# Optimization experiments

Hardware: AMD Instinct MI355X
Metric: run time of the kernel (lower is better)

## Reference

```python
import jax, jax.numpy as jnp
import numpy as np
from jax import lax

IN, H, OUT = 28, 64, 10


def _uniform(key, shape, bound):
    return jax.random.uniform(key, shape, jnp.float32, -bound, bound)


def setup_inputs() -> dict:
    key = jax.random.key(0)
    ks = jax.random.split(key, 11)
    b = 1.0 / np.sqrt(H)  # PyTorch LSTM/Linear init bound
    x = jax.random.normal(ks[0], (2048, 512, IN), jnp.float32)
    return {
        "x": x,
        "W_ih0": _uniform(ks[1], (4 * H, IN), b),
        "W_hh0": _uniform(ks[2], (4 * H, H), b),
        "b_ih0": _uniform(ks[3], (4 * H,), b),
        "b_hh0": _uniform(ks[4], (4 * H,), b),
        "W_ih1": _uniform(ks[5], (4 * H, H), b),
        "W_hh1": _uniform(ks[6], (4 * H, H), b),
        "b_ih1": _uniform(ks[7], (4 * H,), b),
        "b_hh1": _uniform(ks[8], (4 * H,), b),
        "W_out": _uniform(ks[9], (OUT, H), b),
        "b_out": _uniform(ks[10], (OUT,), b),
    }


def _lstm_layer(x_tbd, Wih, Whh, bih, bhh):
    # x_tbd: [T, B, D]; PyTorch gate order: i, f, g, o
    B = x_tbd.shape[1]
    h0 = jnp.zeros((B, H), x_tbd.dtype)
    c0 = jnp.zeros((B, H), x_tbd.dtype)
    bias = bih + bhh

    def step(carry, x_t):
        h, c = carry
        gates = x_t @ Wih.T + h @ Whh.T + bias  # [B, 4H]
        i, f, g, o = jnp.split(gates, 4, axis=-1)
        i = jax.nn.sigmoid(i)
        f = jax.nn.sigmoid(f)
        g = jnp.tanh(g)
        o = jax.nn.sigmoid(o)
        c = f * c + i * g
        h = o * jnp.tanh(c)
        return (h, c), h

    (_, _), hs = lax.scan(step, (h0, c0), x_tbd)
    return hs  # [T, B, H]


def reference(x, W_ih0, W_hh0, b_ih0, b_hh0, W_ih1, W_hh1, b_ih1, b_hh1, W_out, b_out):
    x_tbd = jnp.transpose(x, (1, 0, 2))  # [T, B, IN]
    h1 = _lstm_layer(x_tbd, W_ih0, W_hh0, b_ih0, b_hh0)  # [T, B, H]
    h2 = _lstm_layer(h1, W_ih1, W_hh1, b_ih1, b_hh1)     # [T, B, H]
    r_last = h2[-1]                                      # r_out[:, -1, :] -> [B, H]
    out = r_last @ W_out.T + b_out                       # [B, OUT]
    return out, r_last
```

## Files before the change

### kernel.cpp

```cpp
#include <hip/hip_runtime.h>
#include <stddef.h>

#define NT 512
#define NI 28
#define NH 64
#define BT 8
#define CH 16
#define XPh 36
#define HPh 72
#define NTH 512

typedef _Float16 f16x8 __attribute__((ext_vector_type(8)));
typedef float    f32x4 __attribute__((ext_vector_type(4)));

__device__ __forceinline__ float sigm(float v)  { return __builtin_amdgcn_rcpf(1.f + __expf(-v)); }
__device__ __forceinline__ float tanh_(float v) { return 1.f - 2.f * __builtin_amdgcn_rcpf(__expf(2.f * v) + 1.f); }

__device__ __forceinline__ void bar_lds() {
    asm volatile("s_waitcnt lgkmcnt(0)\n\ts_barrier" ::: "memory");
}

__device__ __forceinline__ size_t gxi(int idx, int n0, int b0) {
    int b   = idx / (CH * 7);
    int rem = idx - b * (CH * 7);
    int t   = rem / 7;
    int w7  = rem - t * 7;
    return ((size_t)(b0 + b) * NT + (n0 + t)) * 7 + w7;
}
__device__ __forceinline__ void xstoreh(_Float16* dst, int idx, float4 v) {
    int b   = idx / (CH * 7);
    int rem = idx - b * (CH * 7);
    int t   = rem / 7;
    int w7  = rem - t * 7;
    _Float16* row = dst + (t * BT + b) * XPh;
    _Float16 tmp[4] = { (_Float16)v.x, (_Float16)v.y, (_Float16)v.z, (_Float16)v.w };
    *(uint2*)(row + 4 * w7) = *(const uint2*)tmp;
}

__global__ __launch_bounds__(NTH, 2)
void lstm2_mfma(const float* __restrict__ x,
                const float* __restrict__ Wih0, const float* __restrict__ Whh0,
                const float* __restrict__ bih0, const float* __restrict__ bhh0,
                const float* __restrict__ Wih1, const float* __restrict__ Whh1,
                const float* __restrict__ bih1, const float* __restrict__ bhh1,
                const float* __restrict__ Wout, const float* __restrict__ bout,
                float* __restrict__ out, float* __restrict__ rlast)
{
    __shared__ __align__(16) _Float16 s_x[2][CH * BT * XPh];
    __shared__ __align__(16) _Float16 s_h0[2][BT * HPh];
    __shared__ __align__(16) _Float16 s_h1[2][BT * HPh];
    __shared__ __align__(16) float    s_hf[BT * NH];

    const int tid = threadIdx.x;
    const int ln  = tid & 63;
    const int wv  = tid >> 6;
    const int lay = wv >> 2;
    const int w4  = wv & 3;
    const int b0  = blockIdx.x * BT;

    const int colB = ln & 15;
    const int kq   = (ln >> 4) * 8;
    const int bA   = ln & 7;
    const int ue   = w4 * 16 + colB;
    const int m0   = (ln >> 4) * 4;
    const int rq   = (ln >= 32) ? 2 : 0;
    const int bm0  = (m0 + rq) & 7;
    const int bm1  = (m0 + rq + 1) & 7;
    const bool hi  = (rq != 0);
    const int off0 = bm0 * HPh + ue;
    const int off1 = bm1 * HPh + ue;

    #pragma unroll 1
    for (int i = tid; i < (int)(sizeof(s_x) / 4); i += NTH) ((int*)s_x)[i] = 0;
    #pragma unroll 1
    for (int i = tid; i < (int)((sizeof(s_h0) + sizeof(s_h1)) / 4); i += NTH) ((int*)s_h0)[i] = 0;
    __syncthreads();
    if (tid < 2 * CH * BT) {
        int buf = tid >> 7, r = tid & 127;
        s_x[buf][r * XPh + 28] = (_Float16)1.0f;
    }

    const float4* xg4 = (const float4*)x;
    {
        float4 v = xg4[gxi(tid, 0, b0)];
        xstoreh(s_x[0], tid, v);
        if (tid < 384) {
            float4 v2 = xg4[gxi(tid + NTH, 0, b0)];
            xstoreh(s_x[0], tid + NTH, v2);
        }
    }
    __syncthreads();

    const f32x4 z4 = { 0.f, 0.f, 0.f, 0.f };
    float cc0 = 0.f, cc1 = 0.f;
    float4 pfA, pfB;

    if (lay == 0) {
        f16x8 B0[4], B1[4], B2[4];
        #pragma unroll
        for (int t = 0; t < 4; ++t) {
            const int g = 64 * t + ue;
            const float bias0 = bih0[g] + bhh0[g];
            #pragma unroll
            for (int j = 0; j < 8; ++j) {
                int k = kq + j;
                float w0 = (k < NI) ? Wih0[g * NI + k] : (k == 28 ? bias0 : 0.f);
                B0[t][j] = (_Float16)w0;
                B1[t][j] = (_Float16)Whh0[g * NH + k];
                B2[t][j] = (_Float16)Whh0[g * NH + 32 + k];
            }
        }
        f32x4 accx[4];
        #pragma unroll 1
        for (int n = 0; n <= NT; ++n) {
            if ((n & 15) == 0 && n + CH < NT) {
                pfA = xg4[gxi(tid, n + CH, b0)];
                if (tid < 384) pfB = xg4[gxi(tid + NTH, n + CH, b0)];
            }
            if (n < NT) {
                if ((n & 15) == 0) {
                    const _Float16* xrow = s_x[(n >> 4) & 1] + ((n & 15) * BT + bA) * XPh;
                    f16x8 Ax = *(const f16x8*)(xrow + kq);
                    #pragma unroll
                    for (int t = 0; t < 4; ++t)
                        accx[t] = __builtin_amdgcn_mfma_f32_16x16x32_f16(Ax, B0[t], z4, 0, 0, 0);
                }
                const _Float16* h0r = s_h0[(n - 1) & 1] + bA * HPh;
                f16x8 A0 = *(const f16x8*)(h0r + kq);
                f16x8 A1 = *(const f16x8*)(h0r + 32 + kq);
                f32x4 acc[4];
                #pragma unroll
                for (int t = 0; t < 4; ++t) {
                    f32x4 a = __builtin_amdgcn_mfma_f32_16x16x32_f16(A0, B1[t], accx[t], 0, 0, 0);
                    acc[t]  = __builtin_amdgcn_mfma_f32_16x16x32_f16(A1, B2[t], a, 0, 0, 0);
                }
                float g00 = hi ? acc[0][2] : acc[0][0];
                float g10 = hi ? acc[1][2] : acc[1][0];
                float g20 = hi ? acc[2][2] : acc[2][0];
                float g30 = hi ? acc[3][2] : acc[3][0];
                float g01 = hi ? acc[0][3] : acc[0][1];
                float g11 = hi ? acc[1][3] : acc[1][1];
                float g21 = hi ? acc[2][3] : acc[2][1];
                float g31 = hi ? acc[3][3] : acc[3][1];
                _Float16* hw = s_h0[n & 1];
                cc0 = sigm(g10) * cc0 + sigm(g00) * tanh_(g20);
                hw[off0] = (_Float16)(sigm(g30) * tanh_(cc0));
                cc1 = sigm(g11) * cc1 + sigm(g01) * tanh_(g21);
                hw[off1] = (_Float16)(sigm(g31) * tanh_(cc1));
                if ((n & 15) != 15 && n + 1 < NT) {
                    const _Float16* xrow2 = s_x[((n + 1) >> 4) & 1] + (((n + 1) & 15) * BT + bA) * XPh;
                    f16x8 Ax2 = *(const f16x8*)(xrow2 + kq);
                    #pragma unroll
                    for (int t = 0; t < 4; ++t)
                        accx[t] = __builtin_amdgcn_mfma_f32_16x16x32_f16(Ax2, B0[t], z4, 0, 0, 0);
                }
            }
            if ((n & 15) == 15 && n + 1 < NT) {
                _Float16* dst = s_x[((n >> 4) + 1) & 1];
                xstoreh(dst, tid, pfA);
                if (tid < 384) xstoreh(dst, tid + NTH, pfB);
            }
            bar_lds();
        }
    } else {
        f16x8 B0[4], B1[4], B2[4], B3[4]; f32x4 bseed[4];
        #pragma unroll
        for (int t = 0; t < 4; ++t) {
            const int g = 64 * t + ue;
            const float bf = bih1[g] + bhh1[g];
            bseed[t] = (f32x4){ bf, bf, bf, bf };
            #pragma unroll
            for (int j = 0; j < 8; ++j) {
                int k = kq + j;
                B0[t][j] = (_Float16)Wih1[g * NH + k];
                B1[t][j] = (_Float16)Wih1[g * NH + 32 + k];
                B2[t][j] = (_Float16)Whh1[g * NH + k];
                B3[t][j] = (_Float16)Whh1[g * NH + 32 + k];
            }
        }
        #pragma unroll 1
        for (int n = 0; n <= NT; ++n) {
            if ((n & 15) == 0 && n + CH < NT) {
                pfA = xg4[gxi(tid, n + CH, b0)];
                if (tid < 384) pfB = xg4[gxi(tid + NTH, n + CH, b0)];
            }
            if (n >= 1) {
                const _Float16* h0r = s_h0[(n - 1) & 1] + bA * HPh;
                const _Float16* h1r = s_h1[n & 1] + bA * HPh;
                f16x8 A0 = *(const f16x8*)(h0r + kq);
                f16x8 A1 = *(const f16x8*)(h0r + 32 + kq);
                f16x8 A2 = *(const f16x8*)(h1r + kq);
                f16x8 A3 = *(const f16x8*)(h1r + 32 + kq);
                f32x4 accp[4], accq[4];
                #pragma unroll
                for (int t = 0; t < 4; ++t) {
                    f32x4 p = __builtin_amdgcn_mfma_f32_16x16x32_f16(A0, B0[t], bseed[t], 0, 0, 0);
                    accp[t] = __builtin_amdgcn_mfma_f32_16x16x32_f16(A1, B1[t], p, 0, 0, 0);
                    f32x4 q = __builtin_amdgcn_mfma_f32_16x16x32_f16(A2, B2[t], z4, 0, 0, 0);
                    accq[t] = __builtin_amdgcn_mfma_f32_16x16x32_f16(A3, B3[t], q, 0, 0, 0);
                }
                float g00 = (hi ? accp[0][2] : accp[0][0]) + (hi ? accq[0][2] : accq[0][0]);
                float g10 = (hi ? accp[1][2] : accp[1][0]) + (hi ? accq[1][2] : accq[1][0]);
                float g20 = (hi ? accp[2][2] : accp[2][0]) + (hi ? accq[2][2] : accq[2][0]);
                float g30 = (hi ? accp[3][2] : accp[3][0]) + (hi ? accq[3][2] : accq[3][0]);
                float g01 = (hi ? accp[0][3] : accp[0][1]) + (hi ? accq[0][3] : accq[0][1]);
                float g11 = (hi ? accp[1][3] : accp[1][1]) + (hi ? accq[1][3] : accq[1][1]);
                float g21 = (hi ? accp[2][3] : accp[2][1]) + (hi ? accq[2][3] : accq[2][1]);
                float g31 = (hi ? accp[3][3] : accp[3][1]) + (hi ? accq[3][3] : accq[3][1]);
                _Float16* hw = s_h1[(n - 1) & 1];
                cc0 = sigm(g10) * cc0 + sigm(g00) * tanh_(g20);
                float h0v = sigm(g30) * tanh_(cc0);
                hw[off0] = (_Float16)h0v;
                cc1 = sigm(g11) * cc1 + sigm(g01) * tanh_(g21);
                float h1v = sigm(g31) * tanh_(cc1);
                hw[off1] = (_Float16)h1v;
                if (n == NT) {
                    rlast[(size_t)(b0 + bm0) * NH + ue] = h0v;
                    rlast[(size_t)(b0 + bm1) * NH + ue] = h1v;
                    s_hf[bm0 * NH + ue] = h0v;
                    s_hf[bm1 * NH + ue] = h1v;
                }
            }
            if ((n & 15) == 15 && n + 1 < NT) {
                _Float16* dst = s_x[((n >> 4) + 1) & 1];
                xstoreh(dst, tid, pfA);
                if (tid < 384) xstoreh(dst, tid + NTH, pfB);
            }
            bar_lds();
        }
    }

    if (tid < BT * 10) {
        int b = tid / 10, o = tid - 10 * (tid / 10);
        float a = bout[o];
        #pragma unroll
        for (int u = 0; u < NH; ++u) a += Wout[o * NH + u] * s_hf[b * NH + u];
        out[(size_t)(b0 + b) * 10 + o] = a;
    }
}

extern "C" void kernel_launch(void* const* d_in, const int* in_sizes, int n_in,
                              void* d_out, int out_size, void* d_ws, size_t ws_size,
                              hipStream_t stream) {
    const float* x    = (const float*)d_in[0];
    const float* Wih0 = (const float*)d_in[1];
    const float* Whh0 = (const float*)d_in[2];
    const float* bih0 = (const float*)d_in[3];
    const float* bhh0 = (const float*)d_in[4];
    const float* Wih1 = (const float*)d_in[5];
    const float* Whh1 = (const float*)d_in[6];
    const float* bih1 = (const float*)d_in[7];
    const float* bhh1 = (const float*)d_in[8];
    const float* Wout = (const float*)d_in[9];
    const float* bout = (const float*)d_in[10];

    const int B = in_sizes[0] / (NT * NI);
    float* out   = (float*)d_out;
    float* rlast = out + (size_t)B * 10;

    dim3 grid(B / BT), block(NTH);
    hipLaunchKernelGGL(lstm2_mfma, grid, block, 0, stream,
                       x, Wih0, Whh0, bih0, bhh0, Wih1, Whh1, bih1, bhh1,
                       Wout, bout, out, rlast);
}
```

Before: 471.1 us.

## Halve batch tile to 4 rows per block and double blocks per CU

```diff
diff --git a/kernel.cpp b/kernel.cpp
--- a/kernel.cpp
+++ b/kernel.cpp
@@ -4,17 +4,22 @@
 #define NT 512
 #define NI 28
 #define NH 64
-#define BT 8
+#define BT 4
 #define CH 16
 #define XPh 36
 #define HPh 72
 #define NTH 512
+#define XLD (CH*BT*7)
 
 typedef _Float16 f16x8 __attribute__((ext_vector_type(8)));
 typedef float    f32x4 __attribute__((ext_vector_type(4)));
 
 __device__ __forceinline__ float sigm(float v)  { return __builtin_amdgcn_rcpf(1.f + __expf(-v)); }
 __device__ __forceinline__ float tanh_(float v) { return 1.f - 2.f * __builtin_amdgcn_rcpf(__expf(2.f * v) + 1.f); }
+
+__device__ __forceinline__ float sel4(f32x4 a, int q) {
+    return q == 0 ? a[0] : (q == 1 ? a[1] : (q == 2 ? a[2] : a[3]));
+}
 
 __device__ __forceinline__ void bar_lds() {
     asm volatile("s_waitcnt lgkmcnt(0)\n\ts_barrier" ::: "memory");
@@ -37,7 +42,7 @@
     *(uint2*)(row + 4 * w7) = *(const uint2*)tmp;
 }
 
-__global__ __launch_bounds__(NTH, 2)
+__global__ __launch_bounds__(NTH, 4)
 void lstm2_mfma(const float* __restrict__ x,
                 const float* __restrict__ Wih0, const float* __restrict__ Whh0,
                 const float* __restrict__ bih0, const float* __restrict__ bhh0,
@@ -59,16 +64,11 @@
     const int b0  = blockIdx.x * BT;
 
     const int colB = ln & 15;
-    const int kq   = (ln >> 4) * 8;
-    const int bA   = ln & 7;
+    const int q    = ln >> 4;
+    const int kq   = q * 8;
+    const int bA   = ln & 3;
     const int ue   = w4 * 16 + colB;
-    const int m0   = (ln >> 4) * 4;
-    const int rq   = (ln >= 32) ? 2 : 0;
-    const int bm0  = (m0 + rq) & 7;
-    const int bm1  = (m0 + rq + 1) & 7;
-    const bool hi  = (rq != 0);
-    const int off0 = bm0 * HPh + ue;
-    const int off1 = bm1 * HPh + ue;
+    const int offh = q * HPh + ue;
 
     #pragma unroll 1
     for (int i = tid; i < (int)(sizeof(s_x) / 4); i += NTH) ((int*)s_x)[i] = 0;
@@ -76,24 +76,20 @@
     for (int i = tid; i < (int)((sizeof(s_h0) + sizeof(s_h1)) / 4); i += NTH) ((int*)s_h0)[i] = 0;
     __syncthreads();
     if (tid < 2 * CH * BT) {
-        int buf = tid >> 7, r = tid & 127;
+        int buf = tid >> 6, r = tid & 63;
         s_x[buf][r * XPh + 28] = (_Float16)1.0f;
     }
 
     const float4* xg4 = (const float4*)x;
-    {
+    if (tid < XLD) {
         float4 v = xg4[gxi(tid, 0, b0)];
         xstoreh(s_x[0], tid, v);
-        if (tid < 384) {
-            float4 v2 = xg4[gxi(tid + NTH, 0, b0)];
-            xstoreh(s_x[0], tid + NTH, v2);
-        }
     }
     __syncthreads();
 
     const f32x4 z4 = { 0.f, 0.f, 0.f, 0.f };
-    float cc0 = 0.f, cc1 = 0.f;
-    float4 pfA, pfB;
+    float cc0 = 0.f;
+    float4 pfA;
 
     if (lay == 0) {
         f16x8 B0[4], B1[4], B2[4];
@@ -113,10 +109,8 @@
         f32x4 accx[4];
         #pragma unroll 1
         for (int n = 0; n <= NT; ++n) {
-            if ((n & 15) == 0 && n + CH < NT) {
+            if ((n & 15) == 0 && n + CH < NT && tid < XLD)
                 pfA = xg4[gxi(tid, n + CH, b0)];
-                if (tid < 384) pfB = xg4[gxi(tid + NTH, n + CH, b0)];
-            }
             if (n < NT) {
                 if ((n & 15) == 0) {
                     const _Float16* xrow = s_x[(n >> 4) & 1] + ((n & 15) * BT + bA) * XPh;
@@ -134,19 +128,12 @@
                     f32x4 a = __builtin_amdgcn_mfma_f32_16x16x32_f16(A0, B1[t], accx[t], 0, 0, 0);
                     acc[t]  = __builtin_amdgcn_mfma_f32_16x16x32_f16(A1, B2[t], a, 0, 0, 0);
                 }
-                float g00 = hi ? acc[0][2] : acc[0][0];
-                float g10 = hi ? acc[1][2] : acc[1][0];
-                float g20 = hi ? acc[2][2] : acc[2][0];
-                float g30 = hi ? acc[3][2] : acc[3][0];
-                float g01 = hi ? acc[0][3] : acc[0][1];
-                float g11 = hi ? acc[1][3] : acc[1][1];
-                float g21 = hi ? acc[2][3] : acc[2][1];
-                float g31 = hi ? acc[3][3] : acc[3][1];
-                _Float16* hw = s_h0[n & 1];
-                cc0 = sigm(g10) * cc0 + sigm(g00) * tanh_(g20);
-                hw[off0] = (_Float16)(sigm(g30) * tanh_(cc0));
-                cc1 = sigm(g11) * cc1 + sigm(g01) * tanh_(g21);
-                hw[off1] = (_Float16)(sigm(g31) * tanh_(cc1));
+                float g0 = sel4(acc[0], q);
+                float g1 = sel4(acc[1], q);
+                float g2 = sel4(acc[2], q);
+                float g3 = sel4(acc[3], q);
+                cc0 = sigm(g1) * cc0 + sigm(g0) * tanh_(g2);
+                s_h0[n & 1][offh] = (_Float16)(sigm(g3) * tanh_(cc0));
                 if ((n & 15) != 15 && n + 1 < NT) {
                     const _Float16* xrow2 = s_x[((n + 1) >> 4) & 1] + (((n + 1) & 15) * BT + bA) * XPh;
                     f16x8 Ax2 = *(const f16x8*)(xrow2 + kq);
@@ -155,11 +142,8 @@
                         accx[t] = __builtin_amdgcn_mfma_f32_16x16x32_f16(Ax2, B0[t], z4, 0, 0, 0);
                 }
             }
-            if ((n & 15) == 15 && n + 1 < NT) {
-                _Float16* dst = s_x[((n >> 4) + 1) & 1];
-                xstoreh(dst, tid, pfA);
-                if (tid < 384) xstoreh(dst, tid + NTH, pfB);
-            }
+            if ((n & 15) == 15 && n + 1 < NT && tid < XLD)
+                xstoreh(s_x[((n >> 4) + 1) & 1], tid, pfA);
             bar_lds();
         }
     } else {
@@ -180,10 +164,8 @@
         }
         #pragma unroll 1
         for (int n = 0; n <= NT; ++n) {
-            if ((n & 15) == 0 && n + CH < NT) {
+            if ((n & 15) == 0 && n + CH < NT && tid < XLD)
                 pfA = xg4[gxi(tid, n + CH, b0)];
-                if (tid < 384) pfB = xg4[gxi(tid + NTH, n + CH, b0)];
-            }
             if (n >= 1) {
                 const _Float16* h0r = s_h0[(n - 1) & 1] + bA * HPh;
                 const _Float16* h1r = s_h1[n & 1] + bA * HPh;
@@ -191,41 +173,28 @@
                 f16x8 A1 = *(const f16x8*)(h0r + 32 + kq);
                 f16x8 A2 = *(const f16x8*)(h1r + kq);
                 f16x8 A3 = *(const f16x8*)(h1r + 32 + kq);
-                f32x4 accp[4], accq[4];
+                f32x4 acc[4];
                 #pragma unroll
                 for (int t = 0; t < 4; ++t) {
-                    f32x4 p = __builtin_amdgcn_mfma_f32_16x16x32_f16(A0, B0[t], bseed[t], 0, 0, 0);
-                    accp[t] = __builtin_amdgcn_mfma_f32_16x16x32_f16(A1, B1[t], p, 0, 0, 0);
-                    f32x4 q = __builtin_amdgcn_mfma_f32_16x16x32_f16(A2, B2[t], z4, 0, 0, 0);
-                    accq[t] = __builtin_amdgcn_mfma_f32_16x16x32_f16(A3, B3[t], q, 0, 0, 0);
-                }
-                float g00 = (hi ? accp[0][2] : accp[0][0]) + (hi ? accq[0][2] : accq[0][0]);
-                float g10 = (hi ? accp[1][2] : accp[1][0]) + (hi ? accq[1][2] : accq[1][0]);
-                float g20 = (hi ? accp[2][2] : accp[2][0]) + (hi ? accq[2][2] : accq[2][0]);
-                float g30 = (hi ? accp[3][2] : accp[3][0]) + (hi ? accq[3][2] : accq[3][0]);
-                float g01 = (hi ? accp[0][3] : accp[0][1]) + (hi ? accq[0][3] : accq[0][1]);
-                float g11 = (hi ? accp[1][3] : accp[1][1]) + (hi ? accq[1][3] : accq[1][1]);
-                float g21 = (hi ? accp[2][3] : accp[2][1]) + (hi ? accq[2][3] : accq[2][1]);
-                float g31 = (hi ? accp[3][3] : accp[3][1]) + (hi ? accq[3][3] : accq[3][1]);
-                _Float16* hw = s_h1[(n - 1) & 1];
-                cc0 = sigm(g10) * cc0 + sigm(g00) * tanh_(g20);
-                float h0v = sigm(g30) * tanh_(cc0);
-                hw[off0] = (_Float16)h0v;
-                cc1 = sigm(g11) * cc1 + sigm(g01) * tanh_(g21);
-                float h1v = sigm(g31) * tanh_(cc1);
-                hw[off1] = (_Float16)h1v;
+                    f32x4 a = __builtin_amdgcn_mfma_f32_16x16x32_f16(A0, B0[t], bseed[t], 0, 0, 0);
+                    a       = __builtin_amdgcn_mfma_f32_16x16x32_f16(A1, B1[t], a, 0, 0, 0);
+                    a       = __builtin_amdgcn_mfma_f32_16x16x32_f16(A2, B2[t], a, 0, 0, 0);
+                    acc[t]  = __builtin_amdgcn_mfma_f32_16x16x32_f16(A3, B3[t], a, 0, 0, 0);
+                }
+                float g0 = sel4(acc[0], q);
+                float g1 = sel4(acc[1], q);
+                float g2 = sel4(acc[2], q);
+                float g3 = sel4(acc[3], q);
+                cc0 = sigm(g1) * cc0 + sigm(g0) * tanh_(g2);
+                float hv = sigm(g3) * tanh_(cc0);
+                s_h1[(n - 1) & 1][offh] = (_Float16)hv;
                 if (n == NT) {
-                    rlast[(size_t)(b0 + bm0) * NH + ue] = h0v;
-                    rlast[(size_t)(b0 + bm1) * NH + ue] = h1v;
-                    s_hf[bm0 * NH + ue] = h0v;
-                    s_hf[bm1 * NH + ue] = h1v;
-                }
-            }
-            if ((n & 15) == 15 && n + 1 < NT) {
-                _Float16* dst = s_x[((n >> 4) + 1) & 1];
-                xstoreh(dst, tid, pfA);
-                if (tid < 384) xstoreh(dst, tid + NTH, pfB);
-            }
+                    rlast[(size_t)(b0 + q) * NH + ue] = hv;
+                    s_hf[q * NH + ue] = hv;
+                }
+            }
+            if ((n & 15) == 15 && n + 1 < NT && tid < XLD)
+                xstoreh(s_x[((n >> 4) + 1) & 1], tid, pfA);
             bar_lds();
         }
     }
```

After: 609.0 us. 1.29x slower.

## Replace per-step block barriers with LDS flag spin-waits between LSTM layers

Applied to the files above, without the earlier changes.

```diff
diff --git a/kernel.cpp b/kernel.cpp
--- a/kernel.cpp
+++ b/kernel.cpp
@@ -9,16 +9,14 @@
 #define XPh 36
 #define HPh 72
 #define NTH 512
+#define XLD (CH*BT*7)
+#define LEAD 4
 
 typedef _Float16 f16x8 __attribute__((ext_vector_type(8)));
 typedef float    f32x4 __attribute__((ext_vector_type(4)));
 
 __device__ __forceinline__ float sigm(float v)  { return __builtin_amdgcn_rcpf(1.f + __expf(-v)); }
 __device__ __forceinline__ float tanh_(float v) { return 1.f - 2.f * __builtin_amdgcn_rcpf(__expf(2.f * v) + 1.f); }
-
-__device__ __forceinline__ void bar_lds() {
-    asm volatile("s_waitcnt lgkmcnt(0)\n\ts_barrier" ::: "memory");
-}
 
 __device__ __forceinline__ size_t gxi(int idx, int n0, int b0) {
     int b   = idx / (CH * 7);
@@ -47,9 +45,10 @@
                 float* __restrict__ out, float* __restrict__ rlast)
 {
     __shared__ __align__(16) _Float16 s_x[2][CH * BT * XPh];
-    __shared__ __align__(16) _Float16 s_h0[2][BT * HPh];
+    __shared__ __align__(16) _Float16 s_h0[LEAD][BT * HPh];
     __shared__ __align__(16) _Float16 s_h1[2][BT * HPh];
     __shared__ __align__(16) float    s_hf[BT * NH];
+    __shared__ __align__(16) int      s_fl[8];
 
     const int tid = threadIdx.x;
     const int ln  = tid & 63;
@@ -73,7 +72,10 @@
     #pragma unroll 1
     for (int i = tid; i < (int)(sizeof(s_x) / 4); i += NTH) ((int*)s_x)[i] = 0;
     #pragma unroll 1
-    for (int i = tid; i < (int)((sizeof(s_h0) + sizeof(s_h1)) / 4); i += NTH) ((int*)s_h0)[i] = 0;
+    for (int i = tid; i < (int)(sizeof(s_h0) / 4); i += NTH) ((int*)s_h0)[i] = 0;
+    #pragma unroll 1
+    for (int i = tid; i < (int)(sizeof(s_h1) / 4); i += NTH) ((int*)s_h1)[i] = 0;
+    if (tid < 8) s_fl[tid] = -1;
     __syncthreads();
     if (tid < 2 * CH * BT) {
         int buf = tid >> 7, r = tid & 127;
@@ -84,7 +86,7 @@
     {
         float4 v = xg4[gxi(tid, 0, b0)];
         xstoreh(s_x[0], tid, v);
-        if (tid < 384) {
+        if (tid < XLD - NTH) {
             float4 v2 = xg4[gxi(tid + NTH, 0, b0)];
             xstoreh(s_x[0], tid + NTH, v2);
         }
@@ -93,7 +95,8 @@
 
     const f32x4 z4 = { 0.f, 0.f, 0.f, 0.f };
     float cc0 = 0.f, cc1 = 0.f;
-    float4 pfA, pfB;
+    volatile int* fl0 = s_fl;
+    volatile int* fl1 = s_fl + 4;
 
     if (lay == 0) {
         f16x8 B0[4], B1[4], B2[4];
@@ -110,57 +113,70 @@
                 B2[t][j] = (_Float16)Whh0[g * NH + 32 + k];
             }
         }
+        float4 pf0, pf1, pf2, pf3;
         f32x4 accx[4];
         #pragma unroll 1
-        for (int n = 0; n <= NT; ++n) {
+        for (int n = 0; n < NT; ++n) {
             if ((n & 15) == 0 && n + CH < NT) {
-                pfA = xg4[gxi(tid, n + CH, b0)];
-                if (tid < 384) pfB = xg4[gxi(tid + NTH, n + CH, b0)];
-            }
-            if (n < NT) {
-                if ((n & 15) == 0) {
-                    const _Float16* xrow = s_x[(n >> 4) & 1] + ((n & 15) * BT + bA) * XPh;
-                    f16x8 Ax = *(const f16x8*)(xrow + kq);
-                    #pragma unroll
-                    for (int t = 0; t < 4; ++t)
-                        accx[t] = __builtin_amdgcn_mfma_f32_16x16x32_f16(Ax, B0[t], z4, 0, 0, 0);
-                }
-                const _Float16* h0r = s_h0[(n - 1) & 1] + bA * HPh;
-                f16x8 A0 = *(const f16x8*)(h0r + kq);
-                f16x8 A1 = *(const f16x8*)(h0r + 32 + kq);
-                f32x4 acc[4];
+                pf0 = xg4[gxi(tid,       n + CH, b0)];
+                pf1 = xg4[gxi(tid + 256, n + CH, b0)];
+                pf2 = xg4[gxi(tid + 512, n + CH, b0)];
+                if (tid < XLD - 768) pf3 = xg4[gxi(tid + 768, n + CH, b0)];
+            }
+            for (;;) {
+                int a0 = fl0[0], a1 = fl0[1], a2 = fl0[2], a3 = fl0[3];
+                int c0 = fl1[0], c1 = fl1[1], c2 = fl1[2], c3 = fl1[3];
+                int mn0 = min(min(a0, a1), min(a2, a3));
+                int mn1 = min(min(c0, c1), min(c2, c3));
+                if (mn0 >= n - 1 && mn1 >= n - LEAD) break;
+                __builtin_amdgcn_s_sleep(1);
+            }
+            asm volatile("" ::: "memory");
+            if ((n & 15) == 0) {
+                const _Float16* xrow = s_x[(n >> 4) & 1] + ((n & 15) * BT + bA) * XPh;
+                f16x8 Ax = *(const f16x8*)(xrow + kq);
                 #pragma unroll
-                for (int t = 0; t < 4; ++t) {
-                    f32x4 a = __builtin_amdgcn_mfma_f32_16x16x32_f16(A0, B1[t], accx[t], 0, 0, 0);
-                    acc[t]  = __builtin_amdgcn_mfma_f32_16x16x32_f16(A1, B2[t], a, 0, 0, 0);
-                }
-                float g00 = hi ? acc[0][2] : acc[0][0];
-                float g10 = hi ? acc[1][2] : acc[1][0];
-                float g20 = hi ? acc[2][2] : acc[2][0];
-                float g30 = hi ? acc[3][2] : acc[3][0];
-                float g01 = hi ? acc[0][3] : acc[0][1];
-                float g11 = hi ? acc[1][3] : acc[1][1];
-                float g21 = hi ? acc[2][3] : acc[2][1];
-                float g31 = hi ? acc[3][3] : acc[3][1];
-                _Float16* hw = s_h0[n & 1];
-                cc0 = sigm(g10) * cc0 + sigm(g00) * tanh_(g20);
-                hw[off0] = (_Float16)(sigm(g30) * tanh_(cc0));
-                cc1 = sigm(g11) * cc1 + sigm(g01) * tanh_(g21);
-                hw[off1] = (_Float16)(sigm(g31) * tanh_(cc1));
-                if ((n & 15) != 15 && n + 1 < NT) {
-                    const _Float16* xrow2 = s_x[((n + 1) >> 4) & 1] + (((n + 1) & 15) * BT + bA) * XPh;
-                    f16x8 Ax2 = *(const f16x8*)(xrow2 + kq);
-                    #pragma unroll
-                    for (int t = 0; t < 4; ++t)
-                        accx[t] = __builtin_amdgcn_mfma_f32_16x16x32_f16(Ax2, B0[t], z4, 0, 0, 0);
-                }
+                for (int t = 0; t < 4; ++t)
+                    accx[t] = __builtin_amdgcn_mfma_f32_16x16x32_f16(Ax, B0[t], z4, 0, 0, 0);
+            }
+            const _Float16* h0r = s_h0[(n - 1) & (LEAD - 1)] + bA * HPh;
+            f16x8 A0 = *(const f16x8*)(h0r + kq);
+            f16x8 A1 = *(const f16x8*)(h0r + 32 + kq);
+            f32x4 acc[4];
+            #pragma unroll
+            for (int t = 0; t < 4; ++t) {
+                f32x4 a = __builtin_amdgcn_mfma_f32_16x16x32_f16(A0, B1[t], accx[t], 0, 0, 0);
+                acc[t]  = __builtin_amdgcn_mfma_f32_16x16x32_f16(A1, B2[t], a, 0, 0, 0);
+            }
+            float g00 = hi ? acc[0][2] : acc[0][0];
+            float g10 = hi ? acc[1][2] : acc[1][0];
+            float g20 = hi ? acc[2][2] : acc[2][0];
+            float g30 = hi ? acc[3][2] : acc[3][0];
+            float g01 = hi ? acc[0][3] : acc[0][1];
+            float g11 = hi ? acc[1][3] : acc[1][1];
+            float g21 = hi ? acc[2][3] : acc[2][1];
+            float g31 = hi ? acc[3][3] : acc[3][1];
+            _Float16* hw = s_h0[n & (LEAD - 1)];
+            cc0 = sigm(g10) * cc0 + sigm(g00) * tanh_(g20);
+            hw[off0] = (_Float16)(sigm(g30) * tanh_(cc0));
+            cc1 = sigm(g11) * cc1 + sigm(g01) * tanh_(g21);
+            hw[off1] = (_Float16)(sigm(g31) * tanh_(cc1));
+            if ((n & 15) != 15 && n + 1 < NT) {
+                const _Float16* xrow2 = s_x[((n + 1) >> 4) & 1] + (((n + 1) & 15) * BT + bA) * XPh;
+                f16x8 Ax2 = *(const f16x8*)(xrow2 + kq);
+                #pragma unroll
+                for (int t = 0; t < 4; ++t)
+                    accx[t] = __builtin_amdgcn_mfma_f32_16x16x32_f16(Ax2, B0[t], z4, 0, 0, 0);
             }
             if ((n & 15) == 15 && n + 1 < NT) {
                 _Float16* dst = s_x[((n >> 4) + 1) & 1];
-                xstoreh(dst, tid, pfA);
-                if (tid < 384) xstoreh(dst, tid + NTH, pfB);
-            }
-            bar_lds();
+                xstoreh(dst, tid,       pf0);
+                xstoreh(dst, tid + 256, pf1);
+                xstoreh(dst, tid + 512, pf2);
+                if (tid < XLD - 768) xstoreh(dst, tid + 768, pf3);
+            }
+            asm volatile("s_waitcnt lgkmcnt(0)" ::: "memory");
+            if (ln == 0) *(volatile int*)&s_fl[w4] = n;
         }
     } else {
         f16x8 B0[4], B1[4], B2[4], B3[4]; f32x4 bseed[4];
@@ -179,56 +195,57 @@
             }
         }
         #pragma unroll 1
-        for (int n = 0; n <= NT; ++n) {
-            if ((n & 15) == 0 && n + CH < NT) {
-                pfA = xg4[gxi(tid, n + CH, b0)];
-                if (tid < 384) pfB = xg4[gxi(tid + NTH, n + CH, b0)];
-            }
-            if (n >= 1) {
-                const _Float16* h0r = s_h0[(n - 1) & 1] + bA * HPh;
-                const _Float16* h1r = s_h1[n & 1] + bA * HPh;
-                f16x8 A0 = *(const f16x8*)(h0r + kq);
-                f16x8 A1 = *(const f16x8*)(h0r + 32 + kq);
-                f16x8 A2 = *(const f16x8*)(h1r + kq);
-                f16x8 A3 = *(const f16x8*)(h1r + 32 + kq);
-                f32x4 accp[4], accq[4];
-                #pragma unroll
-                for (int t = 0; t < 4; ++t) {
-                    f32x4 p = __builtin_amdgcn_mfma_f32_16x16x32_f16(A0, B0[t], bseed[t], 0, 0, 0);
-                    accp[t] = __builtin_amdgcn_mfma_f32_16x16x32_f16(A1, B1[t], p, 0, 0, 0);
-                    f32x4 q = __builtin_amdgcn_mfma_f32_16x16x32_f16(A2, B2[t], z4, 0, 0, 0);
-                    accq[t] = __builtin_amdgcn_mfma_f32_16x16x32_f16(A3, B3[t], q, 0, 0, 0);
-                }
-                float g00 = (hi ? accp[0][2] : accp[0][0]) + (hi ? accq[0][2] : accq[0][0]);
-                float g10 = (hi ? accp[1][2] : accp[1][0]) + (hi ? accq[1][2] : accq[1][0]);
-                float g20 = (hi ? accp[2][2] : accp[2][0]) + (hi ? accq[2][2] : accq[2][0]);
-                float g30 = (hi ? accp[3][2] : accp[3][0]) + (hi ? accq[3][2] : accq[3][0]);
-                float g01 = (hi ? accp[0][3] : accp[0][1]) + (hi ? accq[0][3] : accq[0][1]);
-                float g11 = (hi ? accp[1][3] : accp[1][1]) + (hi ? accq[1][3] : accq[1][1]);
-                float g21 = (hi ? accp[2][3] : accp[2][1]) + (hi ? accq[2][3] : accq[2][1]);
-                float g31 = (hi ? accp[3][3] : accp[3][1]) + (hi ? accq[3][3] : accq[3][1]);
-                _Float16* hw = s_h1[(n - 1) & 1];
-                cc0 = sigm(g10) * cc0 + sigm(g00) * tanh_(g20);
-                float h0v = sigm(g30) * tanh_(cc0);
-                hw[off0] = (_Float16)h0v;
-                cc1 = sigm(g11) * cc1 + sigm(g01) * tanh_(g21);
-                float h1v = sigm(g31) * tanh_(cc1);
-                hw[off1] = (_Float16)h1v;
-                if (n == NT) {
-                    rlast[(size_t)(b0 + bm0) * NH + ue] = h0v;
-                    rlast[(size_t)(b0 + bm1) * NH + ue] = h1v;
-                    s_hf[bm0 * NH + ue] = h0v;
-                    s_hf[bm1 * NH + ue] = h1v;
-                }
-            }
-            if ((n & 15) == 15 && n + 1 < NT) {
-                _Float16* dst = s_x[((n >> 4) + 1) & 1];
-                xstoreh(dst, tid, pfA);
-                if (tid < 384) xstoreh(dst, tid + NTH, pfB);
-            }
-            bar_lds();
-        }
-    }
+        for (int m = 0; m < NT; ++m) {
+            for (;;) {
+                int a0 = fl0[0], a1 = fl0[1], a2 = fl0[2], a3 = fl0[3];
+                int c0 = fl1[0], c1 = fl1[1], c2 = fl1[2], c3 = fl1[3];
+                int mn0 = min(min(a0, a1), min(a2, a3));
+                int mn1 = min(min(c0, c1), min(c2, c3));
+                if (mn0 >= m && mn1 >= m - 1) break;
+                __builtin_amdgcn_s_sleep(1);
+            }
+            asm volatile("" ::: "memory");
+            const _Float16* h0r = s_h0[m & (LEAD - 1)] + bA * HPh;
+            const _Float16* h1r = s_h1[(m + 1) & 1] + bA * HPh;
+            f16x8 A0 = *(const f16x8*)(h0r + kq);
+            f16x8 A1 = *(const f16x8*)(h0r + 32 + kq);
+            f16x8 A2 = *(const f16x8*)(h1r + kq);
+            f16x8 A3 = *(const f16x8*)(h1r + 32 + kq);
+            f32x4 accp[4], accq[4];
+            #pragma unroll
+            for (int t = 0; t < 4; ++t) {
+                f32x4 p = __builtin_amdgcn_mfma_f32_16x16x32_f16(A0, B0[t], bseed[t], 0, 0, 0);
+                accp[t] = __builtin_amdgcn_mfma_f32_16x16x32_f16(A1, B1[t], p, 0, 0, 0);
+                f32x4 qq = __builtin_amdgcn_mfma_f32_16x16x32_f16(A2, B2[t], z4, 0, 0, 0);
+                accq[t] = __builtin_amdgcn_mfma_f32_16x16x32_f16(A3, B3[t], qq, 0, 0, 0);
+            }
+            float g00 = (hi ? accp[0][2] : accp[0][0]) + (hi ? accq[0][2] : accq[0][0]);
+            float g10 = (hi ? accp[1][2] : accp[1][0]) + (hi ? accq[1][2] : accq[1][0]);
+            float g20 = (hi ? accp[2][2] : accp[2][0]) + (hi ? accq[2][2] : accq[2][0]);
+            float g30 = (hi ? accp[3][2] : accp[3][0]) + (hi ? accq[3][2] : accq[3][0]);
+            float g01 = (hi ? accp[0][3] : accp[0][1]) + (hi ? accq[0][3] : accq[0][1]);
+            float g11 = (hi ? accp[1][3] : accp[1][1]) + (hi ? accq[1][3] : accq[1][1]);
+            float g21 = (hi ? accp[2][3] : accp[2][1]) + (hi ? accq[2][3] : accq[2][1]);
+            float g31 = (hi ? accp[3][3] : accp[3][1]) + (hi ? accq[3][3] : accq[3][1]);
+            _Float16* hw = s_h1[m & 1];
+            cc0 = sigm(g10) * cc0 + sigm(g00) * tanh_(g20);
+            float h0v = sigm(g30) * tanh_(cc0);
+            hw[off0] = (_Float16)h0v;
+            cc1 = sigm(g11) * cc1 + sigm(g01) * tanh_(g21);
+            float h1v = sigm(g31) * tanh_(cc1);
+            hw[off1] = (_Float16)h1v;
+            if (m == NT - 1) {
+                rlast[(size_t)(b0 + bm0) * NH + ue] = h0v;
+                rlast[(size_t)(b0 + bm1) * NH + ue] = h1v;
+                s_hf[bm0 * NH + ue] = h0v;
+                s_hf[bm1 * NH + ue] = h1v;
+            }
+            asm volatile("s_waitcnt lgkmcnt(0)" ::: "memory");
+            if (ln == 0) *(volatile int*)&s_fl[4 + w4] = m;
+        }
+    }
+
+    __syncthreads();
 
     if (tid < BT * 10) {
         int b = tid / 10, o = tid - 10 * (tid / 10);
```

Result: slower. 597.1 us (+26.8%).

## Split LSTM step into two barrier phases and move x prefetch to layer-0 warps

Applied to the files above, without the earlier changes.

```diff
diff --git a/kernel.cpp b/kernel.cpp
--- a/kernel.cpp
+++ b/kernel.cpp
@@ -9,6 +9,7 @@
 #define XPh 36
 #define HPh 72
 #define NTH 512
+#define XLD (CH*BT*7)
 
 typedef _Float16 f16x8 __attribute__((ext_vector_type(8)));
 typedef float    f32x4 __attribute__((ext_vector_type(4)));
@@ -73,7 +74,9 @@
     #pragma unroll 1
     for (int i = tid; i < (int)(sizeof(s_x) / 4); i += NTH) ((int*)s_x)[i] = 0;
     #pragma unroll 1
-    for (int i = tid; i < (int)((sizeof(s_h0) + sizeof(s_h1)) / 4); i += NTH) ((int*)s_h0)[i] = 0;
+    for (int i = tid; i < (int)(sizeof(s_h0) / 4); i += NTH) ((int*)s_h0)[i] = 0;
+    #pragma unroll 1
+    for (int i = tid; i < (int)(sizeof(s_h1) / 4); i += NTH) ((int*)s_h1)[i] = 0;
     __syncthreads();
     if (tid < 2 * CH * BT) {
         int buf = tid >> 7, r = tid & 127;
@@ -84,7 +87,7 @@
     {
         float4 v = xg4[gxi(tid, 0, b0)];
         xstoreh(s_x[0], tid, v);
-        if (tid < 384) {
+        if (tid < XLD - NTH) {
             float4 v2 = xg4[gxi(tid + NTH, 0, b0)];
             xstoreh(s_x[0], tid + NTH, v2);
         }
@@ -93,7 +96,6 @@
 
     const f32x4 z4 = { 0.f, 0.f, 0.f, 0.f };
     float cc0 = 0.f, cc1 = 0.f;
-    float4 pfA, pfB;
 
     if (lay == 0) {
         f16x8 B0[4], B1[4], B2[4];
@@ -110,30 +112,29 @@
                 B2[t][j] = (_Float16)Whh0[g * NH + 32 + k];
             }
         }
-        f32x4 accx[4];
+        float4 pf0, pf1, pf2, pf3;
+        f32x4 acc[4];
         #pragma unroll 1
         for (int n = 0; n <= NT; ++n) {
-            if ((n & 15) == 0 && n + CH < NT) {
-                pfA = xg4[gxi(tid, n + CH, b0)];
-                if (tid < 384) pfB = xg4[gxi(tid + NTH, n + CH, b0)];
-            }
             if (n < NT) {
-                if ((n & 15) == 0) {
-                    const _Float16* xrow = s_x[(n >> 4) & 1] + ((n & 15) * BT + bA) * XPh;
-                    f16x8 Ax = *(const f16x8*)(xrow + kq);
-                    #pragma unroll
-                    for (int t = 0; t < 4; ++t)
-                        accx[t] = __builtin_amdgcn_mfma_f32_16x16x32_f16(Ax, B0[t], z4, 0, 0, 0);
-                }
+                if ((n & 15) == 0 && n + CH < NT) {
+                    pf0 = xg4[gxi(tid,       n + CH, b0)];
+                    pf1 = xg4[gxi(tid + 256, n + CH, b0)];
+                    pf2 = xg4[gxi(tid + 512, n + CH, b0)];
+                    if (tid < XLD - 768) pf3 = xg4[gxi(tid + 768, n + CH, b0)];
+                }
+                const _Float16* xrow = s_x[(n >> 4) & 1] + ((n & 15) * BT + bA) * XPh;
+                f16x8 Ax = *(const f16x8*)(xrow + kq);
                 const _Float16* h0r = s_h0[(n - 1) & 1] + bA * HPh;
                 f16x8 A0 = *(const f16x8*)(h0r + kq);
                 f16x8 A1 = *(const f16x8*)(h0r + 32 + kq);
-                f32x4 acc[4];
                 #pragma unroll
                 for (int t = 0; t < 4; ++t) {
-                    f32x4 a = __builtin_amdgcn_mfma_f32_16x16x32_f16(A0, B1[t], accx[t], 0, 0, 0);
+                    f32x4 a = __builtin_amdgcn_mfma_f32_16x16x32_f16(Ax, B0[t], z4, 0, 0, 0);
+                    a       = __builtin_amdgcn_mfma_f32_16x16x32_f16(A0, B1[t], a, 0, 0, 0);
                     acc[t]  = __builtin_amdgcn_mfma_f32_16x16x32_f16(A1, B2[t], a, 0, 0, 0);
                 }
+                bar_lds();
                 float g00 = hi ? acc[0][2] : acc[0][0];
                 float g10 = hi ? acc[1][2] : acc[1][0];
                 float g20 = hi ? acc[2][2] : acc[2][0];
@@ -147,20 +148,18 @@
                 hw[off0] = (_Float16)(sigm(g30) * tanh_(cc0));
                 cc1 = sigm(g11) * cc1 + sigm(g01) * tanh_(g21);
                 hw[off1] = (_Float16)(sigm(g31) * tanh_(cc1));
-                if ((n & 15) != 15 && n + 1 < NT) {
-                    const _Float16* xrow2 = s_x[((n + 1) >> 4) & 1] + (((n + 1) & 15) * BT + bA) * XPh;
-                    f16x8 Ax2 = *(const f16x8*)(xrow2 + kq);
-                    #pragma unroll
-                    for (int t = 0; t < 4; ++t)
-                        accx[t] = __builtin_amdgcn_mfma_f32_16x16x32_f16(Ax2, B0[t], z4, 0, 0, 0);
-                }
-            }
-            if ((n & 15) == 15 && n + 1 < NT) {
-                _Float16* dst = s_x[((n >> 4) + 1) & 1];
-                xstoreh(dst, tid, pfA);
-                if (tid < 384) xstoreh(dst, tid + NTH, pfB);
-            }
-            bar_lds();
+                if ((n & 15) == 15 && n + 1 < NT) {
+                    _Float16* dst = s_x[((n >> 4) + 1) & 1];
+                    xstoreh(dst, tid,       pf0);
+                    xstoreh(dst, tid + 256, pf1);
+                    xstoreh(dst, tid + 512, pf2);
+                    if (tid < XLD - 768) xstoreh(dst, tid + 768, pf3);
+                }
+                bar_lds();
+            } else {
+                bar_lds();
+                bar_lds();
+            }
         }
     } else {
         f16x8 B0[4], B1[4], B2[4], B3[4]; f32x4 bseed[4];
@@ -178,27 +177,11 @@
                 B3[t][j] = (_Float16)Whh1[g * NH + 32 + k];
             }
         }
+        f32x4 accp[4] = { z4, z4, z4, z4 };
+        f32x4 accq[4] = { z4, z4, z4, z4 };
         #pragma unroll 1
         for (int n = 0; n <= NT; ++n) {
-            if ((n & 15) == 0 && n + CH < NT) {
-                pfA = xg4[gxi(tid, n + CH, b0)];
-                if (tid < 384) pfB = xg4[gxi(tid + NTH, n + CH, b0)];
-            }
-            if (n >= 1) {
-                const _Float16* h0r = s_h0[(n - 1) & 1] + bA * HPh;
-                const _Float16* h1r = s_h1[n & 1] + bA * HPh;
-                f16x8 A0 = *(const f16x8*)(h0r + kq);
-                f16x8 A1 = *(const f16x8*)(h0r + 32 + kq);
-                f16x8 A2 = *(const f16x8*)(h1r + kq);
-                f16x8 A3 = *(const f16x8*)(h1r + 32 + kq);
-                f32x4 accp[4], accq[4];
-                #pragma unroll
-                for (int t = 0; t < 4; ++t) {
-                    f32x4 p = __builtin_amdgcn_mfma_f32_16x16x32_f16(A0, B0[t], bseed[t], 0, 0, 0);
-                    accp[t] = __builtin_amdgcn_mfma_f32_16x16x32_f16(A1, B1[t], p, 0, 0, 0);
-                    f32x4 q = __builtin_amdgcn_mfma_f32_16x16x32_f16(A2, B2[t], z4, 0, 0, 0);
-                    accq[t] = __builtin_amdgcn_mfma_f32_16x16x32_f16(A3, B3[t], q, 0, 0, 0);
-                }
+            if (n >= 2) {
                 float g00 = (hi ? accp[0][2] : accp[0][0]) + (hi ? accq[0][2] : accq[0][0]);
                 float g10 = (hi ? accp[1][2] : accp[1][0]) + (hi ? accq[1][2] : accq[1][0]);
                 float g20 = (hi ? accp[2][2] : accp[2][0]) + (hi ? accq[2][2] : accq[2][0]);
@@ -207,28 +190,51 @@
                 float g11 = (hi ? accp[1][3] : accp[1][1]) + (hi ? accq[1][3] : accq[1][1]);
                 float g21 = (hi ? accp[2][3] : accp[2][1]) + (hi ? accq[2][3] : accq[2][1]);
                 float g31 = (hi ? accp[3][3] : accp[3][1]) + (hi ? accq[3][3] : accq[3][1]);
-                _Float16* hw = s_h1[(n - 1) & 1];
+                _Float16* hw = s_h1[(n - 2) & 1];
                 cc0 = sigm(g10) * cc0 + sigm(g00) * tanh_(g20);
-                float h0v = sigm(g30) * tanh_(cc0);
-                hw[off0] = (_Float16)h0v;
+                hw[off0] = (_Float16)(sigm(g30) * tanh_(cc0));
                 cc1 = sigm(g11) * cc1 + sigm(g01) * tanh_(g21);
-                float h1v = sigm(g31) * tanh_(cc1);
-                hw[off1] = (_Float16)h1v;
-                if (n == NT) {
-                    rlast[(size_t)(b0 + bm0) * NH + ue] = h0v;
-                    rlast[(size_t)(b0 + bm1) * NH + ue] = h1v;
-                    s_hf[bm0 * NH + ue] = h0v;
-                    s_hf[bm1 * NH + ue] = h1v;
-                }
-            }
-            if ((n & 15) == 15 && n + 1 < NT) {
-                _Float16* dst = s_x[((n >> 4) + 1) & 1];
-                xstoreh(dst, tid, pfA);
-                if (tid < 384) xstoreh(dst, tid + NTH, pfB);
+                hw[off1] = (_Float16)(sigm(g31) * tanh_(cc1));
             }
             bar_lds();
-        }
-    }
+            if (n >= 1) {
+                const _Float16* h0r = s_h0[(n - 1) & 1] + bA * HPh;
+                const _Float16* h1r = s_h1[(n - 2) & 1] + bA * HPh;
+                f16x8 A0 = *(const f16x8*)(h0r + kq);
+                f16x8 A1 = *(const f16x8*)(h0r + 32 + kq);
+                f16x8 A2 = *(const f16x8*)(h1r + kq);
+                f16x8 A3 = *(const f16x8*)(h1r + 32 + kq);
+                #pragma unroll
+                for (int t = 0; t < 4; ++t) {
+                    f32x4 p = __builtin_amdgcn_mfma_f32_16x16x32_f16(A0, B0[t], bseed[t], 0, 0, 0);
+                    accp[t] = __builtin_amdgcn_mfma_f32_16x16x32_f16(A1, B1[t], p, 0, 0, 0);
+                    f32x4 qq = __builtin_amdgcn_mfma_f32_16x16x32_f16(A2, B2[t], z4, 0, 0, 0);
+                    accq[t] = __builtin_amdgcn_mfma_f32_16x16x32_f16(A3, B3[t], qq, 0, 0, 0);
+                }
+            }
+            bar_lds();
+        }
+        {
+            float g00 = (hi ? accp[0][2] : accp[0][0]) + (hi ? accq[0][2] : accq[0][0]);
+            float g10 = (hi ? accp[1][2] : accp[1][0]) + (hi ? accq[1][2] : accq[1][0]);
+            float g20 = (hi ? accp[2][2] : accp[2][0]) + (hi ? accq[2][2] : accq[2][0]);
+            float g30 = (hi ? accp[3][2] : accp[3][0]) + (hi ? accq[3][2] : accq[3][0]);
+            float g01 = (hi ? accp[0][3] : accp[0][1]) + (hi ? accq[0][3] : accq[0][1]);
+            float g11 = (hi ? accp[1][3] : accp[1][1]) + (hi ? accq[1][3] : accq[1][1]);
+            float g21 = (hi ? accp[2][3] : accp[2][1]) + (hi ? accq[2][3] : accq[2][1]);
+            float g31 = (hi ? accp[3][3] : accp[3][1]) + (hi ? accq[3][3] : accq[3][1]);
+            cc0 = sigm(g10) * cc0 + sigm(g00) * tanh_(g20);
+            float h0v = sigm(g30) * tanh_(cc0);
+            cc1 = sigm(g11) * cc1 + sigm(g01) * tanh_(g21);
+            float h1v = sigm(g31) * tanh_(cc1);
+            rlast[(size_t)(b0 + bm0) * NH + ue] = h0v;
+            rlast[(size_t)(b0 + bm1) * NH + ue] = h1v;
+            s_hf[bm0 * NH + ue] = h0v;
+            s_hf[bm1 * NH + ue] = h1v;
+        }
+    }
+
+    __syncthreads();
 
     if (tid < BT * 10) {
         int b = tid / 10, o = tid - 10 * (tid / 10);
```

Result: slower. 489.8 us (+4.0%).
